# Kernel tuning notes

Hardware: AMD Instinct MI355X
Metric: run time of the kernel (lower is better)

The kernel has to match this reference:

```python
import jax, jax.numpy as jnp
import numpy as np

B, CDD, HIS, T, L, D, K = 64, 5, 100, 30, 3, 256, 10
THRESHOLD = 0.1


def setup_inputs() -> dict:
    key = jax.random.key(0)
    k1, k2, k3, k4 = jax.random.split(key, 4)
    cdd_repr = jax.random.normal(k1, (B, CDD, D), dtype=jnp.float32)
    his_repr = jax.random.normal(k2, (B, HIS, D), dtype=jnp.float32)
    his_embedding = jax.random.normal(k3, (B, HIS, T, L, D), dtype=jnp.float32)
    # xavier_normal init for Linear(D, D)
    W_sel = jax.random.normal(k4, (D, D), dtype=jnp.float32) * np.sqrt(2.0 / (D + D))
    b_sel = jnp.zeros((D,), dtype=jnp.float32)
    return {"cdd_repr": cdd_repr, "his_repr": his_repr,
            "his_embedding": his_embedding, "W_sel": W_sel, "b_sel": b_sel}


def _l2_normalize(x, eps=1e-12):
    # matches torch F.normalize(dim=-1)
    n = jnp.linalg.norm(x, axis=-1, keepdims=True)
    return x / jnp.maximum(n, eps)


def reference(cdd_repr, his_repr, his_embedding, W_sel, b_sel):
    # selectionProject (Linear) + L2 normalize
    cdd_p = _l2_normalize(cdd_repr @ W_sel.T + b_sel)   # [B, CDD, D]
    his_p = _l2_normalize(his_repr @ W_sel.T + b_sel)   # [B, HIS, D]

    # news-level attention scores [B, CDD, HIS]
    attn = jnp.einsum('bcd,bhd->bch', cdd_p, his_p)

    # top-k over history
    attn_topk, idx = jax.lax.top_k(attn, K)             # [B, CDD, K]

    # multi-dim gather of history embeddings -> [B, CDD, K, T, L, D]
    his_activated = his_embedding[jnp.arange(B)[:, None, None], idx]

    # threshold masking: zero out weights below threshold, scale embeddings
    w = jnp.where(attn_topk < THRESHOLD, 0.0, attn_topk)
    his_activated = his_activated * w[:, :, :, None, None, None]

    return his_activated, idx
```

## Files before the change

kernel.cpp:

```cpp
#include <hip/hip_runtime.h>
#include <hip/hip_bf16.h>

#define NB   64
#define NCDD 5
#define NHIS 100
#define ND   256
#define NK   10
#define TLD  23040
#define THRESH 0.1f
#define NEG_INF (-3.402823466e38f)
#define NROWS_HIS 6400
#define NROWS_CDD 320

typedef float f32x4 __attribute__((ext_vector_type(4)));

__global__ __launch_bounds__(256) void proj_norm_all(
    const float* __restrict__ his_repr,
    const float* __restrict__ cdd_repr,
    const float* __restrict__ W,
    const float* __restrict__ bvec,
    float* __restrict__ Yall)
{
    __shared__ float red[4][8];
    const int r0  = blockIdx.x * 8;
    const int tid = threadIdx.x;
    const int sub = tid & 3;
    const int grp = tid >> 2;
    const int wave = tid >> 6, lane = tid & 63;

    const float* __restrict__ X = (r0 < NROWS_HIS)
        ? (his_repr + (size_t)r0 * ND)
        : (cdd_repr + (size_t)(r0 - NROWS_HIS) * ND);

    float acc[4][8];
#pragma unroll
    for (int p = 0; p < 4; ++p)
#pragma unroll
        for (int r = 0; r < 8; ++r) acc[p][r] = 0.f;

#pragma unroll 4
    for (int i = 0; i < 16; ++i) {
        const int kb = sub * 4 + 16 * i;
        float4 x4[8];
#pragma unroll
        for (int r = 0; r < 8; ++r)
            x4[r] = *(const float4*)(X + (size_t)r * ND + kb);
#pragma unroll
        for (int p = 0; p < 4; ++p) {
            const int d = p * 64 + grp;
            const float4 w4 = *(const float4*)(W + (size_t)d * ND + kb);
#pragma unroll
            for (int r = 0; r < 8; ++r)
                acc[p][r] += w4.x * x4[r].x + w4.y * x4[r].y
                           + w4.z * x4[r].z + w4.w * x4[r].w;
        }
    }

#pragma unroll
    for (int p = 0; p < 4; ++p)
#pragma unroll
        for (int r = 0; r < 8; ++r) {
            float v = acc[p][r];
            v += __shfl_xor(v, 1);
            v += __shfl_xor(v, 2);
            acc[p][r] = v;
        }

    float bias[4];
#pragma unroll
    for (int p = 0; p < 4; ++p) bias[p] = bvec[p * 64 + grp];

    float ss[8];
#pragma unroll
    for (int r = 0; r < 8; ++r) {
        float t = 0.f;
#pragma unroll
        for (int p = 0; p < 4; ++p) {
            const float y = acc[p][r] + bias[p];
            acc[p][r] = y;
            t += y * y;
        }
        for (int off = 32; off; off >>= 1) t += __shfl_xor(t, off);
        ss[r] = t;
    }
    if (lane == 0) {
#pragma unroll
        for (int r = 0; r < 8; ++r) red[wave][r] = ss[r];
    }
    __syncthreads();

#pragma unroll
    for (int r = 0; r < 8; ++r) {
        const float s = 0.25f * (red[0][r] + red[1][r] + red[2][r] + red[3][r]);
        const float scale = 1.0f / fmaxf(sqrtf(s), 1e-12f);
        if (sub == 0) {
#pragma unroll
            for (int p = 0; p < 4; ++p)
                Yall[(size_t)(r0 + r) * ND + p * 64 + grp] = acc[p][r] * scale;
        }
    }
}

__global__ __launch_bounds__(256) void attn_gather_kernel(
    const float* __restrict__ cdd_p,
    const float* __restrict__ his_p,
    const float* __restrict__ his_emb,
    float* __restrict__ out_idx_f,
    float* __restrict__ out)
{
    __shared__ float attn_s[128];
    __shared__ float pick_w[NK];
    __shared__ int   pick_i[NK];

    const int orig = blockIdx.x;
    const int g = (orig & 7) * 400 + (orig >> 3);
    const int b = g / (NCDD * NK);
    const int c = (g / NK) % NCDD;
    const int k = g % NK;
    const int tid = threadIdx.x;
    const int sub = tid & 3, grp = tid >> 2;
    const int wave = tid >> 6, lane = tid & 63;

    const float* __restrict__ crow = cdd_p + ((size_t)b * NCDD + c) * ND;
    const float* __restrict__ hbase = his_p + (size_t)b * NHIS * ND;
    {
        const int h0 = grp, h1 = grp + 64;
        const float* __restrict__ h0row = hbase + (size_t)h0 * ND;
        const float* __restrict__ h1row = hbase + (size_t)h1 * ND;
        float a0 = 0.f, a1 = 0.f;
#pragma unroll
        for (int i = 0; i < 16; ++i) {
            const int kb = sub * 4 + 16 * i;
            const float4 cv = *(const float4*)(crow + kb);
            const float4 v0 = *(const float4*)(h0row + kb);
            a0 += cv.x * v0.x + cv.y * v0.y + cv.z * v0.z + cv.w * v0.w;
            if (h1 < NHIS) {
                const float4 v1 = *(const float4*)(h1row + kb);
                a1 += cv.x * v1.x + cv.y * v1.y + cv.z * v1.z + cv.w * v1.w;
            }
        }
        a0 += __shfl_xor(a0, 1); a0 += __shfl_xor(a0, 2);
        a1 += __shfl_xor(a1, 1); a1 += __shfl_xor(a1, 2);
        if (sub == 0) {
            attn_s[h0] = a0;
            if (h1 < NHIS) attn_s[h1] = a1;
        }
    }
    __syncthreads();

    if (wave == 0) {
        float v0 = attn_s[lane];
        float v1 = (lane + 64 < NHIS) ? attn_s[lane + 64] : NEG_INF;
#pragma unroll
        for (int kk = 0; kk < NK; ++kk) {
            float lv; int li;
            if (v1 > v0) { lv = v1; li = lane + 64; }
            else         { lv = v0; li = lane; }
            for (int off = 1; off < 64; off <<= 1) {
                const float ov = __shfl_xor(lv, off);
                const int   oi = __shfl_xor(li, off);
                if (ov > lv || (ov == lv && oi < li)) { lv = ov; li = oi; }
            }
            if (lane == 0) {
                pick_i[kk] = li;
                pick_w[kk] = (lv < THRESH) ? 0.0f : lv;
            }
            if (li == lane)            v0 = NEG_INF;
            else if (li == lane + 64)  v1 = NEG_INF;
        }
    }
    __syncthreads();

    const int   idx = pick_i[k];
    const float w   = pick_w[k];
    if (tid == 0) out_idx_f[g] = (float)idx;

    f32x4* __restrict__ dst = (f32x4*)(out + (size_t)g * TLD);

    if (w == 0.0f) {
        const f32x4 z = {0.f, 0.f, 0.f, 0.f};
#pragma unroll
        for (int it = 0; it < 22; ++it) dst[tid + it * 256] = z;
        if (tid < 128) dst[22 * 256 + tid] = z;
        return;
    }

    const f32x4* __restrict__ src =
        (const f32x4*)(his_emb + ((size_t)b * NHIS + idx) * TLD);

    f32x4 v[22];
    f32x4 vt;
#pragma unroll
    for (int j = 0; j < 22; ++j) v[j] = src[tid + j * 256];
    const bool tail = (tid < 128);
    if (tail) vt = src[22 * 256 + tid];

#pragma unroll
    for (int j = 0; j < 22; ++j) dst[tid + j * 256] = v[j] * w;
    if (tail) dst[22 * 256 + tid] = vt * w;
}

extern "C" void kernel_launch(void* const* d_in, const int* in_sizes, int n_in,
                              void* d_out, int out_size, void* d_ws, size_t ws_size,
                              hipStream_t stream)
{
    const float* cdd_repr = (const float*)d_in[0];
    const float* his_repr = (const float*)d_in[1];
    const float* his_emb  = (const float*)d_in[2];
    const float* W_sel    = (const float*)d_in[3];
    const float* b_sel    = (const float*)d_in[4];
    float* out = (float*)d_out;

    char* ws = (char*)d_ws;
    float* Yall  = (float*)ws;
    float* his_p = Yall;
    float* cdd_p = Yall + (size_t)NROWS_HIS * ND;

    float* out_idx_f = out + (size_t)NB * NCDD * NK * TLD;

    proj_norm_all<<<(NROWS_HIS + NROWS_CDD) / 8, 256, 0, stream>>>(
        his_repr, cdd_repr, W_sel, b_sel, Yall);
    attn_gather_kernel<<<NB * NCDD * NK, 256, 0, stream>>>(
        cdd_p, his_p, his_emb, out_idx_f, out);
}
```

Baseline: 178.3 us.

## Split top-k selection from gather to avoid redundant per-block attention recompute

Each gather block previously recomputed the full 100-entry attention row and top-10 selection for its (b,c) pair, so the work was repeated ten times. A separate kernel now computes the top-k once per (b,c) and writes indices and weights to workspace. A lean gather kernel then reads these and streams the embeddings. This adds an extra kernel launch and a small workspace round trip in exchange for removing the redundant compute from the bandwidth-bound copy path.

```diff
diff --git a/kernel.cpp b/kernel.cpp
--- a/kernel.cpp
+++ b/kernel.cpp
@@ -101,27 +101,21 @@
     }
 }
 
-__global__ __launch_bounds__(256) void attn_gather_kernel(
+__global__ __launch_bounds__(256) void attn_topk_kernel(
     const float* __restrict__ cdd_p,
     const float* __restrict__ his_p,
-    const float* __restrict__ his_emb,
     float* __restrict__ out_idx_f,
-    float* __restrict__ out)
+    int* __restrict__ ws_idx,
+    float* __restrict__ ws_w)
 {
     __shared__ float attn_s[128];
-    __shared__ float pick_w[NK];
-    __shared__ int   pick_i[NK];
-
-    const int orig = blockIdx.x;
-    const int g = (orig & 7) * 400 + (orig >> 3);
-    const int b = g / (NCDD * NK);
-    const int c = (g / NK) % NCDD;
-    const int k = g % NK;
+    const int bc  = blockIdx.x;
+    const int b   = bc / NCDD;
     const int tid = threadIdx.x;
     const int sub = tid & 3, grp = tid >> 2;
     const int wave = tid >> 6, lane = tid & 63;
 
-    const float* __restrict__ crow = cdd_p + ((size_t)b * NCDD + c) * ND;
+    const float* __restrict__ crow = cdd_p + (size_t)bc * ND;
     const float* __restrict__ hbase = his_p + (size_t)b * NHIS * ND;
     {
         const int h0 = grp, h1 = grp + 64;
@@ -152,7 +146,7 @@
         float v0 = attn_s[lane];
         float v1 = (lane + 64 < NHIS) ? attn_s[lane + 64] : NEG_INF;
 #pragma unroll
-        for (int kk = 0; kk < NK; ++kk) {
+        for (int k = 0; k < NK; ++k) {
             float lv; int li;
             if (v1 > v0) { lv = v1; li = lane + 64; }
             else         { lv = v0; li = lane; }
@@ -162,18 +156,29 @@
                 if (ov > lv || (ov == lv && oi < li)) { lv = ov; li = oi; }
             }
             if (lane == 0) {
-                pick_i[kk] = li;
-                pick_w[kk] = (lv < THRESH) ? 0.0f : lv;
+                const float w = (lv < THRESH) ? 0.0f : lv;
+                const int g = bc * NK + k;
+                ws_idx[g] = li;
+                ws_w[g]   = w;
+                out_idx_f[g] = (float)li;
             }
             if (li == lane)            v0 = NEG_INF;
             else if (li == lane + 64)  v1 = NEG_INF;
         }
     }
-    __syncthreads();
-
-    const int   idx = pick_i[k];
-    const float w   = pick_w[k];
-    if (tid == 0) out_idx_f[g] = (float)idx;
+}
+
+__global__ __launch_bounds__(256) void gather_kernel(
+    const float* __restrict__ his_emb,
+    const int* __restrict__ ws_idx,
+    const float* __restrict__ ws_w,
+    float* __restrict__ out)
+{
+    const int orig = blockIdx.x;
+    const int g = (orig & 7) * 400 + (orig >> 3);
+    const int b = g / (NCDD * NK);
+    const int tid = threadIdx.x;
+    const float w = ws_w[g];
 
     f32x4* __restrict__ dst = (f32x4*)(out + (size_t)g * TLD);
 
@@ -185,6 +190,7 @@
         return;
     }
 
+    const int idx = ws_idx[g];
     const f32x4* __restrict__ src =
         (const f32x4*)(his_emb + ((size_t)b * NHIS + idx) * TLD);
 
@@ -215,11 +221,14 @@
     float* Yall  = (float*)ws;
     float* his_p = Yall;
     float* cdd_p = Yall + (size_t)NROWS_HIS * ND;
+    int*   idx_i = (int*)(ws + 6881280);
+    float* w_w   = (float*)(ws + 6894080);
 
     float* out_idx_f = out + (size_t)NB * NCDD * NK * TLD;
 
     proj_norm_all<<<(NROWS_HIS + NROWS_CDD) / 8, 256, 0, stream>>>(
         his_repr, cdd_repr, W_sel, b_sel, Yall);
-    attn_gather_kernel<<<NB * NCDD * NK, 256, 0, stream>>>(
-        cdd_p, his_p, his_emb, out_idx_f, out);
-}
+    attn_topk_kernel<<<NB * NCDD, 256, 0, stream>>>(cdd_p, his_p,
+                                                    out_idx_f, idx_i, w_w);
+    gather_kernel<<<NB * NCDD * NK, 256, 0, stream>>>(his_emb, idx_i, w_w, out);
+}
```

Result: faster. 159.9 us (median of 2 runs) (-10.3%).
